# Kernel tuning notes

Hardware: AMD Instinct MI355X
Metric: run time of the kernel (lower is better)

## Reference

```python
import jax, jax.numpy as jnp
import numpy as np

N = 50000
E = 1600000
EPS = 1e-8  # torch CosineSimilarity eps


def gcn_layer(x, W, b, edge_index, n):
    src, dst = edge_index[0], edge_index[1]
    h = x @ W  # [n, out]
    deg = jnp.ones((n,), x.dtype).at[dst].add(1.0)  # in-degree + self loop
    dinv = jax.lax.rsqrt(deg)
    norm = dinv[src] * dinv[dst]  # [E]
    agg = jnp.zeros_like(h).at[dst].add(norm[:, None] * h[src])
    agg = agg + (dinv * dinv)[:, None] * h  # self-loop term (norm = dinv_i^2)
    return agg + b


def setup_inputs() -> dict:
    key = jax.random.key(0)
    ks = jax.random.split(key, 12)
    drug = jax.random.normal(ks[0], (N, 2048), jnp.float32)
    target = jax.random.normal(ks[1], (N, 1024), jnp.float32)
    drug_edge_index = jax.random.randint(ks[2], (2, E), 0, N)
    target_edge_index = jax.random.randint(ks[3], (2, E), 0, N)
    # projector weights (xavier-ish scale), stored as [in, out]
    Wd = jax.random.normal(ks[4], (2048, 1024), jnp.float32) * np.sqrt(2.0 / (2048 + 1024))
    bd = jnp.zeros((1024,), jnp.float32)
    Wt = jax.random.normal(ks[5], (1024, 1024), jnp.float32) * np.sqrt(2.0 / (1024 + 1024))
    bt = jnp.zeros((1024,), jnp.float32)
    # shared GCN layers (applied to both graphs)
    W1 = jax.random.normal(ks[6], (1024, 512), jnp.float32) * np.sqrt(2.0 / (1024 + 512))
    b1 = jnp.zeros((512,), jnp.float32)
    W2 = jax.random.normal(ks[7], (512, 512), jnp.float32) * np.sqrt(2.0 / (512 + 512))
    b2 = jnp.zeros((512,), jnp.float32)
    return {"drug": drug, "target": target,
            "drug_edge_index": drug_edge_index, "target_edge_index": target_edge_index,
            "Wd": Wd, "bd": bd, "Wt": Wt, "bt": bt,
            "W1": W1, "b1": b1, "W2": W2, "b2": b2}


def reference(drug, target, drug_edge_index, target_edge_index,
              Wd, bd, Wt, bt, W1, b1, W2, b2):
    # projectors: Linear + ReLU
    dp = jax.nn.relu(drug @ Wd + bd)   # [N, 1024]
    tp = jax.nn.relu(target @ Wt + bt)  # [N, 1024]
    # shared GNN layers on each graph
    dp = gcn_layer(dp, W1, b1, drug_edge_index, N)
    tp = gcn_layer(tp, W1, b1, target_edge_index, N)
    dp = gcn_layer(dp, W2, b2, drug_edge_index, N)
    tp = gcn_layer(tp, W2, b2, target_edge_index, N)
    # Cosine similarity along feature dim, then sigmoid
    dn = jnp.maximum(jnp.linalg.norm(dp, axis=1), EPS)
    tn = jnp.maximum(jnp.linalg.norm(tp, axis=1), EPS)
    cos = jnp.sum(dp * tp, axis=1) / (dn * tn)  # [N]
    return jax.nn.sigmoid(cos)
```

## Files before the change

kernel.cpp:

```cpp
#include <hip/hip_runtime.h>
#include <math.h>

#define NNODES 50000
#define NEDGES 1600000
#define MP 50048

typedef unsigned int uint_t;
typedef __attribute__((ext_vector_type(8))) short short8;
typedef __attribute__((ext_vector_type(4))) float f32x4;

__device__ __forceinline__ unsigned short f2bf(float f){
  union { float f; uint_t u; } v; v.f = f;
  uint_t u = v.u;
  uint_t r = (u + 0x7fffu + ((u >> 16) & 1u)) >> 16;
  return (unsigned short)r;
}
__device__ __forceinline__ float bf2f(uint_t u){
  union { uint_t u; float f; } v; v.u = u << 16;
  return v.f;
}

__global__ void k_init_counts(int* cnt_d, int* cnt_t, int n){
  int i = blockIdx.x*blockDim.x + threadIdx.x;
  if (i < n){ cnt_d[i] = 0; cnt_t[i] = 0; }
}

__global__ void k_count(const int* __restrict__ ei, int* __restrict__ cnt, int e){
  int i = blockIdx.x*blockDim.x + threadIdx.x;
  if (i < e) atomicAdd(&cnt[ei[e + i]], 1);
}

__global__ __launch_bounds__(1024) void k_scan(const int* __restrict__ cnt,
    int* __restrict__ rowptr, int* __restrict__ cur, float* __restrict__ dinv, int n){
  __shared__ int sdata[1024];
  __shared__ int s_run;
  const int tid = threadIdx.x;
  if (tid == 0) s_run = 0;
  __syncthreads();
  for (int base = 0; base < n; base += 1024){
    int i = base + tid;
    int v = (i < n) ? cnt[i] : 0;
    sdata[tid] = v;
    __syncthreads();
    for (int off = 1; off < 1024; off <<= 1){
      int t = (tid >= off) ? sdata[tid - off] : 0;
      __syncthreads();
      sdata[tid] += t;
      __syncthreads();
    }
    int excl = sdata[tid] - v;
    int run = s_run;
    if (i < n){
      rowptr[i] = run + excl;
      cur[i]    = run + excl;
      dinv[i]   = 1.0f / sqrtf(1.0f + (float)v);
    }
    __syncthreads();
    if (tid == 1023) s_run = run + sdata[1023];
    __syncthreads();
  }
  if (tid == 0) rowptr[n] = s_run;
}

__global__ void k_fill(const int* __restrict__ ei, int* __restrict__ cur,
                       int* __restrict__ col, float* __restrict__ w,
                       const float* __restrict__ dinv, int e){
  int i = blockIdx.x*blockDim.x + threadIdx.x;
  if (i < e){
    int src = ei[i], dst = ei[e + i];
    int pos = atomicAdd(&cur[dst], 1);
    col[pos] = src;
    w[pos]   = dinv[src];
  }
}

__global__ void k_cast_bf(const float* __restrict__ src, unsigned short* __restrict__ dst,
                          long long n_src, long long n_total){
  long long i = ((long long)blockIdx.x * 256 + threadIdx.x) * 4;
  if (i >= n_total) return;
  ushort4 o;
  if (i < n_src){
    float4 v = *(const float4*)&src[i];
    o.x = f2bf(v.x); o.y = f2bf(v.y); o.z = f2bf(v.z); o.w = f2bf(v.w);
  } else { o.x = 0; o.y = 0; o.z = 0; o.w = 0; }
  *(ushort4*)&dst[i] = o;
}

__global__ __launch_bounds__(256) void k_tr_cast(const float* __restrict__ W,
    unsigned short* __restrict__ WT, int K, int N){
  __shared__ float t[32][33];
  int bx = blockIdx.x * 32;
  int by = blockIdx.y * 32;
  int x = threadIdx.x & 31, y0 = threadIdx.x >> 5;
  for (int y = y0; y < 32; y += 8)
    t[y][x] = W[(size_t)(by + y)*N + bx + x];
  __syncthreads();
  for (int y = y0; y < 32; y += 8)
    WT[(size_t)(bx + y)*K + by + x] = f2bf(t[x][y]);
}

__global__ __launch_bounds__(256) void gemm_bf16(
    const unsigned short* __restrict__ A, const unsigned short* __restrict__ BT,
    const float* __restrict__ bias, void* __restrict__ Cv,
    int N, int K, int relu, int out_bf16)
{
  __shared__ unsigned short As[128*32];
  __shared__ unsigned short Bs[128*32];
  const int tid  = threadIdx.x;
  const int lane = tid & 63;
  const int wave = tid >> 6;
  const long long bm = (long long)blockIdx.y * 128;
  const int bn = blockIdx.x * 128;
  const int wm = (wave & 1) * 64;
  const int wn = (wave >> 1) * 64;
  const int srow = lane >> 2;
  const int sg   = lane & 3;
  const int gcol = (sg ^ ((srow >> 1) & 3)) * 8;
  const unsigned short* pa0 = A  + (bm + wave*32 + srow) * K + gcol;
  const unsigned short* pb0 = BT + (long long)(bn + wave*32 + srow) * K + gcol;
  unsigned short* lA0 = As + (wave*32     )*32;
  unsigned short* lA1 = As + (wave*32 + 16)*32;
  unsigned short* lB0 = Bs + (wave*32     )*32;
  unsigned short* lB1 = Bs + (wave*32 + 16)*32;

  const int lm = lane & 15;
  const int q  = lane >> 4;
  const int fcol = ((q ^ ((lm >> 1) & 3)) * 8);

  f32x4 acc[4][4] = {};

  for (int k0 = 0; k0 < K; k0 += 32){
    __builtin_amdgcn_global_load_lds((const __attribute__((address_space(1))) void*)(pa0 + k0),
        (__attribute__((address_space(3))) void*)lA0, 16, 0, 0);
    __builtin_amdgcn_global_load_lds((const __attribute__((address_space(1))) void*)(pa0 + 16*K + k0),
        (__attribute__((address_space(3))) void*)lA1, 16, 0, 0);
    __builtin_amdgcn_global_load_lds((const __attribute__((address_space(1))) void*)(pb0 + k0),
        (__attribute__((address_space(3))) void*)lB0, 16, 0, 0);
    __builtin_amdgcn_global_load_lds((const __attribute__((address_space(1))) void*)(pb0 + 16*K + k0),
        (__attribute__((address_space(3))) void*)lB1, 16, 0, 0);
    __syncthreads();
    short8 af[4], bfr[4];
    #pragma unroll
    for (int i = 0; i < 4; i++){
      af[i]  = *(const short8*)&As[(wm + 16*i + lm)*32 + fcol];
      bfr[i] = *(const short8*)&Bs[(wn + 16*i + lm)*32 + fcol];
    }
    #pragma unroll
    for (int i = 0; i < 4; i++)
      #pragma unroll
      for (int j = 0; j < 4; j++)
        acc[i][j] = __builtin_amdgcn_mfma_f32_16x16x32_bf16(af[i], bfr[j], acc[i][j], 0, 0, 0);
    __syncthreads();
  }

  #pragma unroll
  for (int j = 0; j < 4; j++){
    int c = bn + wn + 16*j + lm;
    float bv = bias ? bias[c] : 0.f;
    #pragma unroll
    for (int i = 0; i < 4; i++){
      long long mrow = bm + wm + 16*i + q*4;
      #pragma unroll
      for (int r = 0; r < 4; r++){
        float v = acc[i][j][r] + bv;
        if (relu) v = fmaxf(v, 0.f);
        if (out_bf16) ((unsigned short*)Cv)[(mrow + r)*N + c] = f2bf(v);
        else          ((float*)Cv)[(mrow + r)*N + c] = v;
      }
    }
  }
}

__global__ __launch_bounds__(256) void k_agg_bf(
    const unsigned short* __restrict__ H, const int* __restrict__ rowptr,
    const int* __restrict__ col, const float* __restrict__ w,
    const float* __restrict__ dinv, const float* __restrict__ bias,
    unsigned short* __restrict__ out)
{
  const int row = blockIdx.x;
  const int f = threadIdx.x * 2;
  const int beg = rowptr[row], end = rowptr[row+1];
  float ax = 0.f, ay = 0.f;
  for (int e = beg; e < end; e++){
    int s = col[e]; float ws = w[e];
    uint_t h = *(const uint_t*)&H[(size_t)s*512 + f];
    ax += ws * bf2f(h & 0xffffu);
    ay += ws * bf2f(h >> 16);
  }
  float di = dinv[row];
  uint_t hs = *(const uint_t*)&H[(size_t)row*512 + f];
  float ox = di*ax + di*di*bf2f(hs & 0xffffu) + bias[f];
  float oy = di*ay + di*di*bf2f(hs >> 16) + bias[f+1];
  uint_t o = (uint_t)f2bf(ox) | ((uint_t)f2bf(oy) << 16);
  *(uint_t*)&out[(size_t)row*512 + f] = o;
}

__global__ __launch_bounds__(256) void k_cos_bf(const unsigned short* __restrict__ a,
    const unsigned short* __restrict__ b, float* __restrict__ out, int n)
{
  const int lane = threadIdx.x & 63;
  const int wid  = threadIdx.x >> 6;
  const int row  = blockIdx.x*4 + wid;
  if (row >= n) return;
  uint4 x = *(const uint4*)&a[(size_t)row*512 + lane*8];
  uint4 y = *(const uint4*)&b[(size_t)row*512 + lane*8];
  uint_t xs[4] = {x.x, x.y, x.z, x.w};
  uint_t ys[4] = {y.x, y.y, y.z, y.w};
  float dot = 0.f, na = 0.f, nb = 0.f;
  #pragma unroll
  for (int k = 0; k < 4; k++){
    float x0 = bf2f(xs[k] & 0xffffu), x1 = bf2f(xs[k] >> 16);
    float y0 = bf2f(ys[k] & 0xffffu), y1 = bf2f(ys[k] >> 16);
    dot += x0*y0 + x1*y1;
    na  += x0*x0 + x1*x1;
    nb  += y0*y0 + y1*y1;
  }
  #pragma unroll
  for (int off = 32; off; off >>= 1){
    dot += __shfl_down(dot, off);
    na  += __shfl_down(na , off);
    nb  += __shfl_down(nb , off);
  }
  if (lane == 0){
    float dn = fmaxf(sqrtf(na), 1e-8f);
    float tn = fmaxf(sqrtf(nb), 1e-8f);
    out[row] = 1.f/(1.f + expf(-dot/(dn*tn)));
  }
}

extern "C" void kernel_launch(void* const* d_in, const int* in_sizes, int n_in,
                              void* d_out, int out_size, void* d_ws, size_t ws_size,
                              hipStream_t stream)
{
  (void)in_sizes; (void)n_in; (void)out_size; (void)ws_size;
  const float* drug   = (const float*)d_in[0];
  const float* target = (const float*)d_in[1];
  const int*   ei_d   = (const int*)d_in[2];
  const int*   ei_t   = (const int*)d_in[3];
  const float* Wd = (const float*)d_in[4];
  const float* bd = (const float*)d_in[5];
  const float* Wt = (const float*)d_in[6];
  const float* bt = (const float*)d_in[7];
  const float* W1 = (const float*)d_in[8];
  const float* b1 = (const float*)d_in[9];
  const float* W2 = (const float*)d_in[10];
  const float* b2 = (const float*)d_in[11];
  float* out = (float*)d_out;

  const int n = NNODES, E = NEDGES;
  char* ws = (char*)d_ws;
  size_t off = 0;
  auto alloc = [&](size_t bytes)->char* {
    char* p = ws + off; off += (bytes + 255) & ~(size_t)255; return p;
  };
  int*   cnt_d  = (int*)  alloc((size_t)n*4);
  int*   cnt_t  = (int*)  alloc((size_t)n*4);
  int*   rp_d   = (int*)  alloc((size_t)(n+1)*4);
  int*   rp_t   = (int*)  alloc((size_t)(n+1)*4);
  int*   cur_d  = (int*)  alloc((size_t)n*4);
  int*   cur_t  = (int*)  alloc((size_t)n*4);
  int*   col_d  = (int*)  alloc((size_t)E*4);
  int*   col_t  = (int*)  alloc((size_t)E*4);
  float* w_d    = (float*)alloc((size_t)E*4);
  float* w_t    = (float*)alloc((size_t)E*4);
  float* dinv_d = (float*)alloc((size_t)n*4);
  float* dinv_t = (float*)alloc((size_t)n*4);
  unsigned short* WdT = (unsigned short*)alloc((size_t)1024*2048*2);
  unsigned short* WtT = (unsigned short*)alloc((size_t)1024*1024*2);
  unsigned short* W1T = (unsigned short*)alloc((size_t)512*1024*2);
  unsigned short* W2T = (unsigned short*)alloc((size_t)512*512*2);
  unsigned short* bufA = (unsigned short*)alloc((size_t)MP*2048*2);
  unsigned short* bufP = (unsigned short*)alloc((size_t)MP*1024*2);
  unsigned short* bufH = (unsigned short*)alloc((size_t)MP*512*2);
  unsigned short* dp1  = (unsigned short*)alloc((size_t)MP*512*2);
  unsigned short* dp2d = (unsigned short*)alloc((size_t)MP*512*2);
  unsigned short* dp2t = (unsigned short*)alloc((size_t)MP*512*2);

  dim3 blk(256);

  k_init_counts<<<(n+255)/256, blk, 0, stream>>>(cnt_d, cnt_t, n);
  k_count<<<(E+255)/256, blk, 0, stream>>>(ei_d, cnt_d, E);
  k_count<<<(E+255)/256, blk, 0, stream>>>(ei_t, cnt_t, E);
  k_scan<<<1, 1024, 0, stream>>>(cnt_d, rp_d, cur_d, dinv_d, n);
  k_scan<<<1, 1024, 0, stream>>>(cnt_t, rp_t, cur_t, dinv_t, n);
  k_fill<<<(E+255)/256, blk, 0, stream>>>(ei_d, cur_d, col_d, w_d, dinv_d, E);
  k_fill<<<(E+255)/256, blk, 0, stream>>>(ei_t, cur_t, col_t, w_t, dinv_t, E);

  k_tr_cast<<<dim3(1024/32, 2048/32), blk, 0, stream>>>(Wd, WdT, 2048, 1024);
  k_tr_cast<<<dim3(1024/32, 1024/32), blk, 0, stream>>>(Wt, WtT, 1024, 1024);
  k_tr_cast<<<dim3( 512/32, 1024/32), blk, 0, stream>>>(W1, W1T, 1024,  512);
  k_tr_cast<<<dim3( 512/32,  512/32), blk, 0, stream>>>(W2, W2T,  512,  512);

  {
    long long nsrc = (long long)n*2048, ntot = (long long)MP*2048;
    k_cast_bf<<<(unsigned)((ntot/4 + 255)/256), blk, 0, stream>>>(drug, bufA, nsrc, ntot);
  }
  gemm_bf16<<<dim3(8, MP/128), blk, 0, stream>>>(bufA, WdT, bd, bufP, 1024, 2048, 1, 1);
  gemm_bf16<<<dim3(4, MP/128), blk, 0, stream>>>(bufP, W1T, nullptr, bufH, 512, 1024, 0, 1);
  k_agg_bf<<<n, blk, 0, stream>>>(bufH, rp_d, col_d, w_d, dinv_d, b1, dp1);
  gemm_bf16<<<dim3(4, MP/128), blk, 0, stream>>>(dp1, W2T, nullptr, bufH, 512, 512, 0, 1);
  k_agg_bf<<<n, blk, 0, stream>>>(bufH, rp_d, col_d, w_d, dinv_d, b2, dp2d);

  {
    long long nsrc = (long long)n*1024, ntot = (long long)MP*1024;
    k_cast_bf<<<(unsigned)((ntot/4 + 255)/256), blk, 0, stream>>>(target, bufA, nsrc, ntot);
  }
  gemm_bf16<<<dim3(8, MP/128), blk, 0, stream>>>(bufA, WtT, bt, bufP, 1024, 1024, 1, 1);
  gemm_bf16<<<dim3(4, MP/128), blk, 0, stream>>>(bufP, W1T, nullptr, bufH, 512, 1024, 0, 1);
  k_agg_bf<<<n, blk, 0, stream>>>(bufH, rp_t, col_t, w_t, dinv_t, b1, dp1);
  gemm_bf16<<<dim3(4, MP/128), blk, 0, stream>>>(dp1, W2T, nullptr, bufH, 512, 512, 0, 1);
  k_agg_bf<<<n, blk, 0, stream>>>(bufH, rp_t, col_t, w_t, dinv_t, b2, dp2t);

  k_cos_bf<<<(n+3)/4, blk, 0, stream>>>(dp2d, dp2t, out, n);
}
```

Measured before the change: 3.383 ms.

## Parallelize scan, batch both graphs in shared GEMMs, XCD-remap tiles, widen aggregation

Replaces the single-block serial CSR scan with a three-kernel multi-block scan covering both graphs at once. Drug and target features are stacked so the W1 and W2 GEMMs each run as one double-height launch. GEMM workgroups are remapped so consecutive tiles land on the same XCD, aiming for better L2 reuse. The aggregation kernel now handles two rows per block with 4-wide feature loads and a 4-way unrolled edge loop for more memory-level parallelism. Buffers are reused (dp1 aliases bufP, dp2 aliases bufA), which adds aliasing risk.

```diff
diff --git a/kernel.cpp b/kernel.cpp
--- a/kernel.cpp
+++ b/kernel.cpp
@@ -30,36 +30,68 @@
   if (i < e) atomicAdd(&cnt[ei[e + i]], 1);
 }
 
-__global__ __launch_bounds__(1024) void k_scan(const int* __restrict__ cnt,
-    int* __restrict__ rowptr, int* __restrict__ cur, float* __restrict__ dinv, int n){
+__global__ __launch_bounds__(1024) void k_scan_blk(
+    const int* __restrict__ cnt_d, const int* __restrict__ cnt_t,
+    int* __restrict__ rp_d, int* __restrict__ rp_t,
+    float* __restrict__ dinv_d, float* __restrict__ dinv_t,
+    int* __restrict__ bsum, int n)
+{
+  const int g = blockIdx.y;
+  const int* cnt = g ? cnt_t : cnt_d;
+  int* rp        = g ? rp_t  : rp_d;
+  float* dinv    = g ? dinv_t: dinv_d;
   __shared__ int sdata[1024];
-  __shared__ int s_run;
   const int tid = threadIdx.x;
-  if (tid == 0) s_run = 0;
+  const int i = blockIdx.x*1024 + tid;
+  int v = (i < n) ? cnt[i] : 0;
+  sdata[tid] = v;
   __syncthreads();
-  for (int base = 0; base < n; base += 1024){
-    int i = base + tid;
-    int v = (i < n) ? cnt[i] : 0;
-    sdata[tid] = v;
+  for (int off = 1; off < 1024; off <<= 1){
+    int t = (tid >= off) ? sdata[tid - off] : 0;
     __syncthreads();
-    for (int off = 1; off < 1024; off <<= 1){
-      int t = (tid >= off) ? sdata[tid - off] : 0;
-      __syncthreads();
-      sdata[tid] += t;
-      __syncthreads();
-    }
-    int excl = sdata[tid] - v;
-    int run = s_run;
-    if (i < n){
-      rowptr[i] = run + excl;
-      cur[i]    = run + excl;
-      dinv[i]   = 1.0f / sqrtf(1.0f + (float)v);
-    }
+    sdata[tid] += t;
     __syncthreads();
-    if (tid == 1023) s_run = run + sdata[1023];
-    __syncthreads();
-  }
-  if (tid == 0) rowptr[n] = s_run;
+  }
+  if (i < n){
+    rp[i]   = sdata[tid] - v;
+    dinv[i] = 1.0f / sqrtf(1.0f + (float)v);
+  }
+  if (tid == 1023) bsum[g*64 + blockIdx.x] = sdata[1023];
+}
+
+__global__ __launch_bounds__(128) void k_scan_bsum(
+    int* __restrict__ bsum, int* __restrict__ rp_d, int* __restrict__ rp_t,
+    int nb, int n)
+{
+  const int g = threadIdx.x >> 6;
+  const int lane = threadIdx.x & 63;
+  int orig = (lane < nb) ? bsum[g*64 + lane] : 0;
+  int v = orig;
+  #pragma unroll
+  for (int off = 1; off < 64; off <<= 1){
+    int t = __shfl_up(v, off);
+    if (lane >= off) v += t;
+  }
+  if (lane < nb) bsum[g*64 + lane] = v - orig;
+  if (lane == nb-1){
+    if (g) rp_t[n] = v; else rp_d[n] = v;
+  }
+}
+
+__global__ __launch_bounds__(1024) void k_scan_add(
+    const int* __restrict__ bsum,
+    int* __restrict__ rp_d, int* __restrict__ rp_t,
+    int* __restrict__ cur_d, int* __restrict__ cur_t, int n)
+{
+  const int g = blockIdx.y;
+  int* rp  = g ? rp_t  : rp_d;
+  int* cur = g ? cur_t : cur_d;
+  const int i = blockIdx.x*1024 + threadIdx.x;
+  if (i < n){
+    int v = rp[i] + bsum[g*64 + blockIdx.x];
+    rp[i] = v;
+    cur[i] = v;
+  }
 }
 
 __global__ void k_fill(const int* __restrict__ ei, int* __restrict__ cur,
@@ -109,8 +141,17 @@
   const int tid  = threadIdx.x;
   const int lane = tid & 63;
   const int wave = tid >> 6;
-  const long long bm = (long long)blockIdx.y * 128;
-  const int bn = blockIdx.x * 128;
+
+  const int gx  = gridDim.x;
+  const int nwg = gx * gridDim.y;
+  const int id  = blockIdx.y * gx + blockIdx.x;
+  const int q = nwg >> 3, r = nwg & 7;
+  const int xcd = id & 7, rank = id >> 3;
+  const int nid = (xcd < r) ? (xcd*(q+1) + rank)
+                            : (r*(q+1) + (xcd - r)*q + rank);
+  const long long bm = (long long)(nid / gx) * 128;
+  const int bn = (nid % gx) * 128;
+
   const int wm = (wave & 1) * 64;
   const int wn = (wave >> 1) * 64;
   const int srow = lane >> 2;
@@ -124,8 +165,8 @@
   unsigned short* lB1 = Bs + (wave*32 + 16)*32;
 
   const int lm = lane & 15;
-  const int q  = lane >> 4;
-  const int fcol = ((q ^ ((lm >> 1) & 3)) * 8);
+  const int q2 = lane >> 4;
+  const int fcol = ((q2 ^ ((lm >> 1) & 3)) * 8);
 
   f32x4 acc[4][4] = {};
 
@@ -159,13 +200,13 @@
     float bv = bias ? bias[c] : 0.f;
     #pragma unroll
     for (int i = 0; i < 4; i++){
-      long long mrow = bm + wm + 16*i + q*4;
+      long long mrow = bm + wm + 16*i + q2*4;
       #pragma unroll
-      for (int r = 0; r < 4; r++){
-        float v = acc[i][j][r] + bv;
+      for (int rr = 0; rr < 4; rr++){
+        float v = acc[i][j][rr] + bv;
         if (relu) v = fmaxf(v, 0.f);
-        if (out_bf16) ((unsigned short*)Cv)[(mrow + r)*N + c] = f2bf(v);
-        else          ((float*)Cv)[(mrow + r)*N + c] = v;
+        if (out_bf16) ((unsigned short*)Cv)[(mrow + rr)*N + c] = f2bf(v);
+        else          ((float*)Cv)[(mrow + rr)*N + c] = v;
       }
     }
   }
@@ -175,24 +216,50 @@
     const unsigned short* __restrict__ H, const int* __restrict__ rowptr,
     const int* __restrict__ col, const float* __restrict__ w,
     const float* __restrict__ dinv, const float* __restrict__ bias,
-    unsigned short* __restrict__ out)
-{
-  const int row = blockIdx.x;
-  const int f = threadIdx.x * 2;
+    unsigned short* __restrict__ out, int nrows)
+{
+  const int half = threadIdx.x >> 7;
+  const int t    = threadIdx.x & 127;
+  const int row  = blockIdx.x*2 + half;
+  if (row >= nrows) return;
+  const int f = t * 4;
   const int beg = rowptr[row], end = rowptr[row+1];
-  float ax = 0.f, ay = 0.f;
-  for (int e = beg; e < end; e++){
+  float a0 = 0.f, a1 = 0.f, a2 = 0.f, a3 = 0.f;
+  int e = beg;
+  for (; e + 3 < end; e += 4){
+    int s0 = col[e], s1 = col[e+1], s2 = col[e+2], s3 = col[e+3];
+    float w0 = w[e], w1 = w[e+1], w2 = w[e+2], w3 = w[e+3];
+    uint2 h0 = *(const uint2*)&H[(size_t)s0*512 + f];
+    uint2 h1 = *(const uint2*)&H[(size_t)s1*512 + f];
+    uint2 h2 = *(const uint2*)&H[(size_t)s2*512 + f];
+    uint2 h3 = *(const uint2*)&H[(size_t)s3*512 + f];
+    a0 += w0*bf2f(h0.x & 0xffffu) + w1*bf2f(h1.x & 0xffffu)
+        + w2*bf2f(h2.x & 0xffffu) + w3*bf2f(h3.x & 0xffffu);
+    a1 += w0*bf2f(h0.x >> 16)     + w1*bf2f(h1.x >> 16)
+        + w2*bf2f(h2.x >> 16)     + w3*bf2f(h3.x >> 16);
+    a2 += w0*bf2f(h0.y & 0xffffu) + w1*bf2f(h1.y & 0xffffu)
+        + w2*bf2f(h2.y & 0xffffu) + w3*bf2f(h3.y & 0xffffu);
+    a3 += w0*bf2f(h0.y >> 16)     + w1*bf2f(h1.y >> 16)
+        + w2*bf2f(h2.y >> 16)     + w3*bf2f(h3.y >> 16);
+  }
+  for (; e < end; ++e){
     int s = col[e]; float ws = w[e];
-    uint_t h = *(const uint_t*)&H[(size_t)s*512 + f];
-    ax += ws * bf2f(h & 0xffffu);
-    ay += ws * bf2f(h >> 16);
+    uint2 h = *(const uint2*)&H[(size_t)s*512 + f];
+    a0 += ws*bf2f(h.x & 0xffffu); a1 += ws*bf2f(h.x >> 16);
+    a2 += ws*bf2f(h.y & 0xffffu); a3 += ws*bf2f(h.y >> 16);
   }
   float di = dinv[row];
-  uint_t hs = *(const uint_t*)&H[(size_t)row*512 + f];
-  float ox = di*ax + di*di*bf2f(hs & 0xffffu) + bias[f];
-  float oy = di*ay + di*di*bf2f(hs >> 16) + bias[f+1];
-  uint_t o = (uint_t)f2bf(ox) | ((uint_t)f2bf(oy) << 16);
-  *(uint_t*)&out[(size_t)row*512 + f] = o;
+  float sc = di*di;
+  uint2 hs = *(const uint2*)&H[(size_t)row*512 + f];
+  float4 bv = *(const float4*)&bias[f];
+  float o0 = di*a0 + sc*bf2f(hs.x & 0xffffu) + bv.x;
+  float o1 = di*a1 + sc*bf2f(hs.x >> 16)     + bv.y;
+  float o2 = di*a2 + sc*bf2f(hs.y & 0xffffu) + bv.z;
+  float o3 = di*a3 + sc*bf2f(hs.y >> 16)     + bv.w;
+  uint2 o;
+  o.x = (uint_t)f2bf(o0) | ((uint_t)f2bf(o1) << 16);
+  o.y = (uint_t)f2bf(o2) | ((uint_t)f2bf(o3) << 16);
+  *(uint2*)&out[(size_t)row*512 + f] = o;
 }
 
 __global__ __launch_bounds__(256) void k_cos_bf(const unsigned short* __restrict__ a,
@@ -265,24 +332,26 @@
   float* w_t    = (float*)alloc((size_t)E*4);
   float* dinv_d = (float*)alloc((size_t)n*4);
   float* dinv_t = (float*)alloc((size_t)n*4);
+  int*   bsum   = (int*)  alloc(128*4);
   unsigned short* WdT = (unsigned short*)alloc((size_t)1024*2048*2);
   unsigned short* WtT = (unsigned short*)alloc((size_t)1024*1024*2);
   unsigned short* W1T = (unsigned short*)alloc((size_t)512*1024*2);
   unsigned short* W2T = (unsigned short*)alloc((size_t)512*512*2);
   unsigned short* bufA = (unsigned short*)alloc((size_t)MP*2048*2);
-  unsigned short* bufP = (unsigned short*)alloc((size_t)MP*1024*2);
-  unsigned short* bufH = (unsigned short*)alloc((size_t)MP*512*2);
-  unsigned short* dp1  = (unsigned short*)alloc((size_t)MP*512*2);
-  unsigned short* dp2d = (unsigned short*)alloc((size_t)MP*512*2);
-  unsigned short* dp2t = (unsigned short*)alloc((size_t)MP*512*2);
+  unsigned short* bufP = (unsigned short*)alloc((size_t)2*MP*1024*2);
+  unsigned short* bufH = (unsigned short*)alloc((size_t)2*MP*512*2);
+  unsigned short* dp1 = bufP;
+  unsigned short* dp2 = bufA;
 
   dim3 blk(256);
+  const int NB = (n + 1023)/1024;
 
   k_init_counts<<<(n+255)/256, blk, 0, stream>>>(cnt_d, cnt_t, n);
   k_count<<<(E+255)/256, blk, 0, stream>>>(ei_d, cnt_d, E);
   k_count<<<(E+255)/256, blk, 0, stream>>>(ei_t, cnt_t, E);
-  k_scan<<<1, 1024, 0, stream>>>(cnt_d, rp_d, cur_d, dinv_d, n);
-  k_scan<<<1, 1024, 0, stream>>>(cnt_t, rp_t, cur_t, dinv_t, n);
+  k_scan_blk<<<dim3(NB,2), 1024, 0, stream>>>(cnt_d, cnt_t, rp_d, rp_t, dinv_d, dinv_t, bsum, n);
+  k_scan_bsum<<<1, 128, 0, stream>>>(bsum, rp_d, rp_t, NB, n);
+  k_scan_add<<<dim3(NB,2), 1024, 0, stream>>>(bsum, rp_d, rp_t, cur_d, cur_t, n);
   k_fill<<<(E+255)/256, blk, 0, stream>>>(ei_d, cur_d, col_d, w_d, dinv_d, E);
   k_fill<<<(E+255)/256, blk, 0, stream>>>(ei_t, cur_t, col_t, w_t, dinv_t, E);
 
@@ -296,20 +365,21 @@
     k_cast_bf<<<(unsigned)((ntot/4 + 255)/256), blk, 0, stream>>>(drug, bufA, nsrc, ntot);
   }
   gemm_bf16<<<dim3(8, MP/128), blk, 0, stream>>>(bufA, WdT, bd, bufP, 1024, 2048, 1, 1);
-  gemm_bf16<<<dim3(4, MP/128), blk, 0, stream>>>(bufP, W1T, nullptr, bufH, 512, 1024, 0, 1);
-  k_agg_bf<<<n, blk, 0, stream>>>(bufH, rp_d, col_d, w_d, dinv_d, b1, dp1);
-  gemm_bf16<<<dim3(4, MP/128), blk, 0, stream>>>(dp1, W2T, nullptr, bufH, 512, 512, 0, 1);
-  k_agg_bf<<<n, blk, 0, stream>>>(bufH, rp_d, col_d, w_d, dinv_d, b2, dp2d);
-
   {
     long long nsrc = (long long)n*1024, ntot = (long long)MP*1024;
     k_cast_bf<<<(unsigned)((ntot/4 + 255)/256), blk, 0, stream>>>(target, bufA, nsrc, ntot);
   }
-  gemm_bf16<<<dim3(8, MP/128), blk, 0, stream>>>(bufA, WtT, bt, bufP, 1024, 1024, 1, 1);
-  gemm_bf16<<<dim3(4, MP/128), blk, 0, stream>>>(bufP, W1T, nullptr, bufH, 512, 1024, 0, 1);
-  k_agg_bf<<<n, blk, 0, stream>>>(bufH, rp_t, col_t, w_t, dinv_t, b1, dp1);
-  gemm_bf16<<<dim3(4, MP/128), blk, 0, stream>>>(dp1, W2T, nullptr, bufH, 512, 512, 0, 1);
-  k_agg_bf<<<n, blk, 0, stream>>>(bufH, rp_t, col_t, w_t, dinv_t, b2, dp2t);
-
-  k_cos_bf<<<(n+3)/4, blk, 0, stream>>>(dp2d, dp2t, out, n);
-}
+  gemm_bf16<<<dim3(8, MP/128), blk, 0, stream>>>(bufA, WtT, bt, bufP + (size_t)MP*1024, 1024, 1024, 1, 1);
+
+  gemm_bf16<<<dim3(4, (2*MP)/128), blk, 0, stream>>>(bufP, W1T, nullptr, bufH, 512, 1024, 0, 1);
+  k_agg_bf<<<(n+1)/2, blk, 0, stream>>>(bufH, rp_d, col_d, w_d, dinv_d, b1, dp1, n);
+  k_agg_bf<<<(n+1)/2, blk, 0, stream>>>(bufH + (size_t)MP*512, rp_t, col_t, w_t, dinv_t, b1,
+                                        dp1 + (size_t)MP*512, n);
+
+  gemm_bf16<<<dim3(4, (2*MP)/128), blk, 0, stream>>>(dp1, W2T, nullptr, bufH, 512, 512, 0, 1);
+  k_agg_bf<<<(n+1)/2, blk, 0, stream>>>(bufH, rp_d, col_d, w_d, dinv_d, b2, dp2, n);
+  k_agg_bf<<<(n+1)/2, blk, 0, stream>>>(bufH + (size_t)MP*512, rp_t, col_t, w_t, dinv_t, b2,
+                                        dp2 + (size_t)MP*512, n);
+
+  k_cos_bf<<<(n+3)/4, blk, 0, stream>>>(dp2, dp2 + (size_t)MP*512, out, n);
+}
```

After: 2.757 ms. -18.5%, faster.
